# Kernel tuning notes

Measured on AMD Instinct MI355X. Metric: run time of the kernel, lower is better.

The kernel has to match this reference:

```python
import jax, jax.numpy as jnp
import numpy as np

EMB = 256

def setup_inputs() -> dict:
    key = jax.random.key(0)
    ks = jax.random.split(key, 7)
    c = EMB
    x = jax.random.normal(ks[0], (4, c, 64, 64), dtype=jnp.float32)
    s = 1.0 / np.sqrt(c)
    Wq = jax.random.uniform(ks[1], (c, c), jnp.float32, -s, s)
    bq = jax.random.uniform(ks[2], (c,), jnp.float32, -s, s)
    Wk = jax.random.uniform(ks[3], (c, c), jnp.float32, -s, s)
    bk = jax.random.uniform(ks[4], (c,), jnp.float32, -s, s)
    Wv = jax.random.uniform(ks[5], (c, c), jnp.float32, -s, s)
    bv = jax.random.uniform(ks[6], (c,), jnp.float32, -s, s)
    return {"x": x, "Wq": Wq, "bq": bq, "Wk": Wk, "bk": bk, "Wv": Wv, "bv": bv}

def reference(x, Wq, bq, Wk, bk, Wv, bv):
    b, c, h, w = x.shape
    scale = jnp.sqrt(jnp.float32(c))
    # [b, n, c] tokens, n = h*w
    xt = x.reshape(b, c, h * w).transpose(0, 2, 1)
    q = jnp.einsum('bnc,dc->bnd', xt, Wq) + bq
    k = jnp.einsum('bnc,dc->bnd', xt, Wk) + bk
    v = jnp.einsum('bnc,dc->bnd', xt, Wv) + bv
    dist = jnp.einsum('bnd,bmd->bnm', q, k) / scale  # [b, n, n]
    dist = jax.nn.softmax(dist, axis=-1)
    mem = jnp.einsum('bnm,bmd->bnd', dist, v)  # [b, n, c]
    # Original: permute(0,1,2) is identity, then raw view(b,c,h,w) -> reshape
    return mem.reshape(b, c, h, w)
```

## Files before the change

kernel.cpp:

```cpp
#include <hip/hip_runtime.h>

typedef __attribute__((ext_vector_type(8))) short short8;
typedef __attribute__((ext_vector_type(4))) short short4_t;
typedef __attribute__((ext_vector_type(4))) float float4_t;
typedef __attribute__((ext_vector_type(16))) float float16_t;
typedef __attribute__((ext_vector_type(2))) int int2_t;

#define NTOK 4096
#define CDIM 256
#define BPB (NTOK * CDIM)
#define C1 0.0901684400555602f

__device__ inline float bf2f(short s) {
    return __uint_as_float(((unsigned)(unsigned short)s) << 16);
}
__device__ inline short f2bf(float f) {
    unsigned u = __float_as_uint(f);
    return (short)((u + 0x7fffu + ((u >> 16) & 1u)) >> 16);
}
__device__ inline int cvtpk_bf16(float lo, float hi) {
    int d;
    asm("v_cvt_pk_bf16_f32 %0, %1, %2" : "=v"(d) : "v"(lo), "v"(hi));
    return d;
}
__device__ inline void gl_lds16(const void* g, void* l) {
    __builtin_amdgcn_global_load_lds(
        (const __attribute__((address_space(1))) unsigned int*)g,
        (__attribute__((address_space(3))) unsigned int*)l, 16, 0, 0);
}

__global__ void sniff_dtype(const unsigned* __restrict__ x, int* __restrict__ flag) {
    __shared__ int cnt;
    if (threadIdx.x == 0) cnt = 0;
    __syncthreads();
    int local = 0;
    for (int i = threadIdx.x; i < 1024; i += 256) {
        unsigned e = (x[i] >> 7) & 0xffu;
        if (e >= 100u && e <= 140u) local++;
    }
    atomicAdd(&cnt, local);
    __syncthreads();
    if (threadIdx.x == 0) flag[0] = (cnt >= 512) ? 1 : 0;
}

__global__ __launch_bounds__(256) void wprep(
    const void* __restrict__ Wq, const void* __restrict__ Wk,
    const void* __restrict__ Wv, const int* __restrict__ flag,
    short* __restrict__ Wb)
{
    const int base = (blockIdx.x * 256 + threadIdx.x) * 8;
    const int wsel = base >> 16, off = base & 65535;
    const void* W = (wsel == 0) ? Wq : (wsel == 1) ? Wk : Wv;
    short8 v;
    if (flag[0]) {
        v = *(const short8*)((const short*)W + off);
    } else {
        const float* f = (const float*)W + off;
        float4 a = *(const float4*)f;
        float4 c4 = *(const float4*)(f + 4);
        v[0]=f2bf(a.x);  v[1]=f2bf(a.y);  v[2]=f2bf(a.z);  v[3]=f2bf(a.w);
        v[4]=f2bf(c4.x); v[5]=f2bf(c4.y); v[6]=f2bf(c4.z); v[7]=f2bf(c4.w);
    }
    *(short8*)(Wb + base) = v;
}

template <bool PIN>
__global__ __launch_bounds__(256, 4) void qkv8(
    const void* __restrict__ xv, const short* __restrict__ Wb,
    const void* __restrict__ bq, const void* __restrict__ bk,
    const void* __restrict__ bv,
    const int* __restrict__ flag, int b0,
    short* __restrict__ qbase, short* __restrict__ kbase,
    short* __restrict__ vtbase)
{
    int nt, bl, wsel;
    if (PIN) {
        const int bid = blockIdx.x;
        wsel = bid >> 8;
        const int rem = bid & 255;
        bl = rem & 3; nt = rem >> 2;
    } else { nt = blockIdx.x; wsel = blockIdx.y; bl = blockIdx.z; }
    const int b = b0 + bl;
    const int n0 = nt * 64;
    const int tid = threadIdx.x;
    const int w = tid >> 6, lane = tid & 63, l15 = lane & 15, qd = lane >> 4;
    const int isbf = flag[0];

    __shared__ short obuf[64 * 264];

    short8 af[8];
    {
        const int n = n0 + 16 * w + l15;
        if (isbf) {
            const short* xs = (const short*)xv + (size_t)b * (CDIM * NTOK) + n;
            #pragma unroll
            for (int s = 0; s < 8; ++s) {
                short8 v;
                #pragma unroll
                for (int e = 0; e < 8; ++e)
                    v[e] = xs[(s * 32 + qd * 8 + e) * NTOK];
                af[s] = v;
            }
        } else {
            const float* xf = (const float*)xv + (size_t)b * (CDIM * NTOK) + n;
            #pragma unroll
            for (int s = 0; s < 8; ++s) {
                short8 v;
                #pragma unroll
                for (int e = 0; e < 8; ++e)
                    v[e] = f2bf(xf[(s * 32 + qd * 8 + e) * NTOK]);
                af[s] = v;
            }
        }
    }

    const short* W = Wb + wsel * 65536;
    const void* bp = (wsel == 0) ? bq : (wsel == 1) ? bk : bv;

    short8 wv[8], wn[8];
    {
        const short* wr = W + l15 * 256 + qd * 8;
        #pragma unroll
        for (int s = 0; s < 8; ++s) wv[s] = *(const short8*)(wr + s * 32);
    }
    #pragma unroll 1
    for (int dg = 0; dg < 16; ++dg) {
        const int d = dg * 16 + l15;
        if (dg + 1 < 16) {
            const short* wr = W + (dg * 16 + 16 + l15) * 256 + qd * 8;
            #pragma unroll
            for (int s = 0; s < 8; ++s) wn[s] = *(const short8*)(wr + s * 32);
        }
        float4_t acc = {0.f, 0.f, 0.f, 0.f};
        #pragma unroll
        for (int s = 0; s < 8; ++s)
            acc = __builtin_amdgcn_mfma_f32_16x16x32_bf16(af[s], wv[s], acc, 0, 0, 0);
        const float bias = isbf ? bf2f(((const short*)bp)[d])
                                : ((const float*)bp)[d];
        if (wsel < 2) {
            #pragma unroll
            for (int r = 0; r < 4; ++r)
                obuf[(16 * w + 4 * qd + r) * 264 + d] = f2bf(acc[r] + bias);
        } else {
            #pragma unroll
            for (int r = 0; r < 4; ++r)
                obuf[d * 66 + (16 * w + 4 * qd + r)] = f2bf(acc[r] + bias);
        }
        #pragma unroll
        for (int s = 0; s < 8; ++s) wv[s] = wn[s];
    }
    __syncthreads();

    if (wsel == 0) {
        short* qdst = qbase + (size_t)bl * BPB;
        const int rl = tid >> 2;
        #pragma unroll
        for (int u = 0; u < 8; ++u) {
            const int cc = (tid & 3) + 4 * u;
            short8 vv = *(const short8*)&obuf[rl * 264 + cc * 8];
            *(short8*)(qdst + (size_t)(n0 + rl) * 256 + cc * 8) = vv;
        }
    } else if (wsel == 1) {
        short* kdst = kbase + (size_t)bl * BPB;
        const int rl = tid >> 2;
        const int tile = (n0 + rl) >> 5, rit = rl & 31;
        #pragma unroll
        for (int u = 0; u < 8; ++u) {
            const int ccp = (tid & 3) + 4 * u;
            const int cc  = ccp ^ rit;
            short8 vv = *(const short8*)&obuf[rl * 264 + cc * 8];
            *(short8*)(kdst + (size_t)tile * 8192 + rit * 256 + ccp * 8) = vv;
        }
    } else {
        short* vtdst = vtbase + (size_t)bl * BPB;
        const int d = tid;
        #pragma unroll
        for (int u = 0; u < 8; ++u) {
            short8 vv = *(const short8*)&obuf[d * 66 + u * 8];
            const int tile = (n0 >> 5) + (u >> 2), ck = u & 3;
            const int pos = ((d & 1) * 4 + ck) ^ ((d >> 1) & 7);
            *(short8*)(vtdst + (size_t)tile * 8192 + (d >> 1) * 64 + pos * 8) = vv;
        }
    }
}

__global__ __launch_bounds__(256, 2) void flash13(
    const short* __restrict__ qb, const short* __restrict__ kb,
    const short* __restrict__ vtb,
    float* __restrict__ pO, float* __restrict__ pl)
{
    const int bid = blockIdx.x;
    const int bl = bid & 3, half = (bid >> 2) & 3, qt = bid >> 4;
    const int q0 = qt * 128;
    const int tid = threadIdx.x;
    const int w = tid >> 6, lane = tid & 63, l31 = lane & 31, h = lane >> 5;

    __shared__ __align__(16) char smem[65536];
    short* kbufA = (short*)smem;
    short* vbufA = (short*)(smem + 32768);

    const short* Q  = qb  + (size_t)bl * BPB;
    const char*  Kc = (const char*)(kb  + (size_t)bl * BPB);
    const char*  Vc = (const char*)(vtb + (size_t)bl * BPB);

    short8 qf[16];
    {
        const short* qrow = Q + (size_t)(q0 + 32 * w + l31) * 256 + h * 8;
        #pragma unroll
        for (int s = 0; s < 16; ++s)
            qf[s] = *(const short8*)(qrow + s * 16);
    }

    float16_t oacc[8];
    #pragma unroll
    for (int dt = 0; dt < 8; ++dt)
        #pragma unroll
        for (int r = 0; r < 16; ++r) oacc[dt][r] = 0.f;
    float ll0 = 0.f, ll1 = 0.f, ll2 = 0.f, ll3 = 0.f;

    const int KT0 = half * 32, KT1 = KT0 + 32;

    {
        const char* ks = Kc + ((size_t)KT0 << 14);
        const char* vs = Vc + ((size_t)KT0 << 14);
        char* kd = smem + tid * 16;
        char* vd = smem + 32768 + tid * 16;
        #pragma unroll
        for (int u = 0; u < 4; ++u) {
            gl_lds16(ks + u * 4096 + tid * 16, kd + u * 4096);
            gl_lds16(vs + u * 4096 + tid * 16, vd + u * 4096);
        }
    }

    float16_t se, so;
    #pragma unroll
    for (int r = 0; r < 16; ++r) { se[r] = 0.f; so[r] = 0.f; }
    short8 pa0, pa1;

    #pragma unroll 1
    for (int kt = KT0; kt < KT1; ++kt) {
        if (kt > KT0) {
            #pragma unroll
            for (int r = 0; r < 16; ++r) se[r] = exp2f((se[r] + so[r]) * C1);
            #pragma unroll
            for (int g = 0; g < 4; ++g) {
                ll0 += se[4 * g + 0]; ll1 += se[4 * g + 1];
                ll2 += se[4 * g + 2]; ll3 += se[4 * g + 3];
            }
            {
                int x0 = cvtpk_bf16(se[0], se[1]);
                int y0 = cvtpk_bf16(se[4], se[5]);
                int z0 = cvtpk_bf16(se[2], se[3]);
                int u0 = cvtpk_bf16(se[6], se[7]);
                int2_t r1 = __builtin_amdgcn_permlane32_swap(x0, y0, false, false);
                int2_t r2 = __builtin_amdgcn_permlane32_swap(z0, u0, false, false);
                union { int i[4]; short8 s8; } uu;
                uu.i[0] = r1[0]; uu.i[1] = r2[0]; uu.i[2] = r1[1]; uu.i[3] = r2[1];
                pa0 = uu.s8;
                int x1 = cvtpk_bf16(se[8],  se[9]);
                int y1 = cvtpk_bf16(se[12], se[13]);
                int z1 = cvtpk_bf16(se[10], se[11]);
                int u1 = cvtpk_bf16(se[14], se[15]);
                int2_t r3 = __builtin_amdgcn_permlane32_swap(x1, y1, false, false);
                int2_t r4 = __builtin_amdgcn_permlane32_swap(z1, u1, false, false);
                union { int i[4]; short8 s8; } vv;
                vv.i[0] = r3[0]; vv.i[1] = r4[0]; vv.i[2] = r3[1]; vv.i[3] = r4[1];
                pa1 = vv.s8;
            }
            {
                const short* vprev = vbufA + ((kt + 1) & 1) * 8192;
                __builtin_amdgcn_s_setprio(1);
                #pragma unroll
                for (int dt = 0; dt < 8; ++dt) {
                    const int d = 32 * dt + l31, d2 = d >> 1;
                    {
                        const int pos = (((d & 1) * 4 + h) ^ (d2 & 7));
                        short8 vf = *(const short8*)&vprev[d2 * 64 + pos * 8];
                        oacc[dt] = __builtin_amdgcn_mfma_f32_32x32x16_bf16(pa0, vf, oacc[dt], 0, 0, 0);
                    }
                    {
                        const int pos = (((d & 1) * 4 + 2 + h) ^ (d2 & 7));
                        short8 vf = *(const short8*)&vprev[d2 * 64 + pos * 8];
                        oacc[dt] = __builtin_amdgcn_mfma_f32_32x32x16_bf16(pa1, vf, oacc[dt], 0, 0, 0);
                    }
                }
                __builtin_amdgcn_s_setprio(0);
            }
        }

        asm volatile("s_waitcnt vmcnt(0) lgkmcnt(0)" ::: "memory");
        __builtin_amdgcn_sched_barrier(0);
        __builtin_amdgcn_s_barrier();
        __builtin_amdgcn_sched_barrier(0);

        if (kt + 1 < KT1) {
            const int alt = (kt + 1) & 1;
            const char* ks = Kc + ((size_t)(kt + 1) << 14);
            const char* vs = Vc + ((size_t)(kt + 1) << 14);
            char* kd = smem + alt * 16384 + tid * 16;
            char* vd = smem + 32768 + alt * 16384 + tid * 16;
            #pragma unroll
            for (int u = 0; u < 4; ++u) {
                gl_lds16(ks + u * 4096 + tid * 16, kd + u * 4096);
                gl_lds16(vs + u * 4096 + tid * 16, vd + u * 4096);
            }
        }

        {
            const short* kcur = kbufA + (kt & 1) * 8192;
            #pragma unroll
            for (int r = 0; r < 16; ++r) { se[r] = 0.f; so[r] = 0.f; }
            __builtin_amdgcn_s_setprio(1);
            #pragma unroll
            for (int j = 0; j < 8; ++j) {
                short8 ka = *(const short8*)
                    &kcur[l31 * 256 + (((4 * j + h) ^ l31) * 8)];
                se = __builtin_amdgcn_mfma_f32_32x32x16_bf16(ka, qf[2 * j], se, 0, 0, 0);
                short8 kb2 = *(const short8*)
                    &kcur[l31 * 256 + (((4 * j + 2 + h) ^ l31) * 8)];
                so = __builtin_amdgcn_mfma_f32_32x32x16_bf16(kb2, qf[2 * j + 1], so, 0, 0, 0);
            }
            __builtin_amdgcn_s_setprio(0);
        }
    }

    {
        #pragma unroll
        for (int r = 0; r < 16; ++r) se[r] = exp2f((se[r] + so[r]) * C1);
        #pragma unroll
        for (int g = 0; g < 4; ++g) {
            ll0 += se[4 * g + 0]; ll1 += se[4 * g + 1];
            ll2 += se[4 * g + 2]; ll3 += se[4 * g + 3];
        }
        int x0 = cvtpk_bf16(se[0], se[1]);
        int y0 = cvtpk_bf16(se[4], se[5]);
        int z0 = cvtpk_bf16(se[2], se[3]);
        int u0 = cvtpk_bf16(se[6], se[7]);
        int2_t r1 = __builtin_amdgcn_permlane32_swap(x0, y0, false, false);
        int2_t r2 = __builtin_amdgcn_permlane32_swap(z0, u0, false, false);
        union { int i[4]; short8 s8; } uu;
        uu.i[0] = r1[0]; uu.i[1] = r2[0]; uu.i[2] = r1[1]; uu.i[3] = r2[1];
        pa0 = uu.s8;
        int x1 = cvtpk_bf16(se[8],  se[9]);
        int y1 = cvtpk_bf16(se[12], se[13]);
        int z1 = cvtpk_bf16(se[10], se[11]);
        int u1 = cvtpk_bf16(se[14], se[15]);
        int2_t r3 = __builtin_amdgcn_permlane32_swap(x1, y1, false, false);
        int2_t r4 = __builtin_amdgcn_permlane32_swap(z1, u1, false, false);
        union { int i[4]; short8 s8; } vv;
        vv.i[0] = r3[0]; vv.i[1] = r4[0]; vv.i[2] = r3[1]; vv.i[3] = r4[1];
        pa1 = vv.s8;

        const short* vlast = vbufA + ((KT1 - 1) & 1) * 8192;
        #pragma unroll
        for (int dt = 0; dt < 8; ++dt) {
            const int d = 32 * dt + l31, d2 = d >> 1;
            {
                const int pos = (((d & 1) * 4 + h) ^ (d2 & 7));
                short8 vf = *(const short8*)&vlast[d2 * 64 + pos * 8];
                oacc[dt] = __builtin_amdgcn_mfma_f32_32x32x16_bf16(pa0, vf, oacc[dt], 0, 0, 0);
            }
            {
                const int pos = (((d & 1) * 4 + 2 + h) ^ (d2 & 7));
                short8 vf = *(const short8*)&vlast[d2 * 64 + pos * 8];
                oacc[dt] = __builtin_amdgcn_mfma_f32_32x32x16_bf16(pa1, vf, oacc[dt], 0, 0, 0);
            }
        }
    }

    const size_t idx = (size_t)(bl * 32 + qt) * 4 + half;
    {
        float v2 = (ll0 + ll1) + (ll2 + ll3);
        v2 += __shfl_xor(v2, 32, 64);
        if (h == 0) pl[idx * 128 + 32 * w + l31] = v2;
    }
    float* po = pO + idx * 32768;
    #pragma unroll
    for (int dt = 0; dt < 8; ++dt) {
        #pragma unroll
        for (int r = 0; r < 16; ++r) {
            const int qrow = 32 * w + (r & 3) + 8 * (r >> 2) + 4 * h;
            po[qrow * 256 + 32 * dt + l31] = oacc[dt][r];
        }
    }
}

__global__ __launch_bounds__(256) void combine4(
    const float* __restrict__ pO, const float* __restrict__ pl,
    const int* __restrict__ flag, void* __restrict__ outv)
{
    const int tid = threadIdx.x, w = tid >> 6, lane = tid & 63;
    const int isbf = flag[0];
    #pragma unroll 1
    for (int st = 0; st < 16; ++st) {
        const int row = blockIdx.x * 64 + st * 4 + w;
        const int bl = row >> 12, n = row & 4095;
        const int qt = n >> 7, prow = n & 127;
        const size_t bidx = (size_t)(bl * 32 + qt) * 4;
        const float* P0 = pO + bidx * 32768 + prow * 256 + lane * 4;
        float4 a = *(const float4*)P0;
        float4 b = *(const float4*)(P0 + 32768);
        float4 c = *(const float4*)(P0 + 65536);
        float4 d = *(const float4*)(P0 + 98304);
        const float inv = 1.0f /
            (pl[(bidx + 0) * 128 + prow] + pl[(bidx + 1) * 128 + prow] +
             pl[(bidx + 2) * 128 + prow] + pl[(bidx + 3) * 128 + prow]);
        float4 r;
        r.x = (a.x + b.x + c.x + d.x) * inv;
        r.y = (a.y + b.y + c.y + d.y) * inv;
        r.z = (a.z + b.z + c.z + d.z) * inv;
        r.w = (a.w + b.w + c.w + d.w) * inv;
        const size_t o = (size_t)row * 256 + lane * 4;
        if (isbf) {
            short4_t pk;
            pk[0] = f2bf(r.x); pk[1] = f2bf(r.y);
            pk[2] = f2bf(r.z); pk[3] = f2bf(r.w);
            *(short4_t*)((short*)outv + o) = pk;
        } else {
            *(float4*)((float*)outv + o) = r;
        }
    }
}

template <bool PIN, bool SPLIT>
__global__ __launch_bounds__(256, 2) void flash12(
    int b0, const short* __restrict__ qb, const short* __restrict__ kb,
    const short* __restrict__ vtb, const int* __restrict__ flag,
    void* __restrict__ outv, float* __restrict__ pO, float* __restrict__ pl)
{
    int qt, bl, half;
    if (SPLIT) {
        const int bid = blockIdx.x;
        bl = (bid >> 1) & 3; half = bid & 1; qt = bid >> 3;
    } else if (PIN) {
        bl = blockIdx.x & 3; qt = blockIdx.x >> 2; half = 0;
    } else { qt = blockIdx.x; bl = blockIdx.z; half = 0; }

    const int b = b0 + bl;
    const int q0 = qt * 64;
    const int tid = threadIdx.x;
    const int w = tid >> 6, lane = tid & 63, l31 = lane & 31, h = lane >> 5;
    const int wi = w & 1, wh = w >> 1;

    __shared__ __align__(16) char smem[67584];
    short* kbufA = (short*)smem;
    short* vbufA = (short*)(smem + 32768);
    float* lbuf  = (float*)(smem + 66560);

    const short* Q  = qb  + (size_t)bl * BPB;
    const char*  Kc = (const char*)(kb  + (size_t)bl * BPB);
    const char*  Vc = (const char*)(vtb + (size_t)bl * BPB);

    short8 qf[16];
    {
        const short* qrow = Q + (size_t)(q0 + 32 * wh + l31) * 256 + h * 8;
        #pragma unroll
        for (int s = 0; s < 16; ++s)
            qf[s] = *(const short8*)(qrow + s * 16);
    }

    float16_t oacc[4];
    #pragma unroll
    for (int dt = 0; dt < 4; ++dt)
        #pragma unroll
        for (int r = 0; r < 16; ++r) oacc[dt][r] = 0.f;
    float ll0 = 0.f, ll1 = 0.f, ll2 = 0.f, ll3 = 0.f;

    const int KT0 = SPLIT ? half * 64 : 0;
    const int KT1 = KT0 + (SPLIT ? 64 : 128);

    {
        const char* ks = Kc + ((size_t)KT0 << 14);
        const char* vs = Vc + ((size_t)KT0 << 14);
        char* kd = smem + tid * 16;
        char* vd = smem + 32768 + tid * 16;
        #pragma unroll
        for (int u = 0; u < 4; ++u) {
            gl_lds16(ks + u * 4096 + tid * 16, kd + u * 4096);
            gl_lds16(vs + u * 4096 + tid * 16, vd + u * 4096);
        }
    }
    __syncthreads();

    short8 pa0 = {0,0,0,0,0,0,0,0}, pa1 = {0,0,0,0,0,0,0,0};

    #pragma unroll 1
    for (int kt = KT0; kt < KT1; ++kt) {
        short* kcur  = kbufA + (kt & 1) * 8192;
        short* vprev = vbufA + ((kt + 1) & 1) * 8192;

        if (kt + 1 < KT1) {
            const char* ks = Kc + ((size_t)(kt + 1) << 14);
            char* kd = smem + (((kt + 1) & 1) << 14) + tid * 16;
            #pragma unroll
            for (int u = 0; u < 4; ++u)
                gl_lds16(ks + u * 4096 + tid * 16, kd + u * 4096);
        }

        float16_t se, so;
        #pragma unroll
        for (int r = 0; r < 16; ++r) { se[r] = 0.f; so[r] = 0.f; }
        #pragma unroll
        for (int j = 0; j < 8; ++j) {
            short8 ka = *(const short8*)
                &kcur[l31 * 256 + (((4 * j + h) ^ l31) * 8)];
            se = __builtin_amdgcn_mfma_f32_32x32x16_bf16(ka, qf[2 * j], se, 0, 0, 0);
            short8 kb2 = *(const short8*)
                &kcur[l31 * 256 + (((4 * j + 2 + h) ^ l31) * 8)];
            so = __builtin_amdgcn_mfma_f32_32x32x16_bf16(kb2, qf[2 * j + 1], so, 0, 0, 0);
        }

        if (kt > KT0) {
            #pragma unroll
            for (int dt = 0; dt < 4; ++dt) {
                const int d = 128 * wi + 32 * dt + l31, d2 = d >> 1;
                {
                    const int pos = (((d & 1) * 4 + h) ^ (d2 & 7));
                    short8 vf = *(const short8*)&vprev[d2 * 64 + pos * 8];
                    oacc[dt] = __builtin_amdgcn_mfma_f32_32x32x16_bf16(pa0, vf, oacc[dt], 0, 0, 0);
                }
                {
                    const int pos = (((d & 1) * 4 + 2 + h) ^ (d2 & 7));
                    short8 vf = *(const short8*)&vprev[d2 * 64 + pos * 8];
                    oacc[dt] = __builtin_amdgcn_mfma_f32_32x32x16_bf16(pa1, vf, oacc[dt], 0, 0, 0);
                }
            }
        }

        asm volatile("s_waitcnt lgkmcnt(0)" ::: "memory");
        __builtin_amdgcn_sched_barrier(0);
        __builtin_amdgcn_s_barrier();
        __builtin_amdgcn_sched_barrier(0);

        if (kt + 1 < KT1) {
            const char* vs = Vc + ((size_t)(kt + 1) << 14);
            char* vd = smem + 32768 + (((kt + 1) & 1) << 14) + tid * 16;
            #pragma unroll
            for (int u = 0; u < 4; ++u)
                gl_lds16(vs + u * 4096 + tid * 16, vd + u * 4096);
        }

        float pf[16];
        #pragma unroll
        for (int r = 0; r < 16; ++r) pf[r] = exp2f((se[r] + so[r]) * C1);
        #pragma unroll
        for (int g = 0; g < 4; ++g) {
            ll0 += pf[4 * g + 0]; ll1 += pf[4 * g + 1];
            ll2 += pf[4 * g + 2]; ll3 += pf[4 * g + 3];
        }
        {
            int x0 = cvtpk_bf16(pf[0], pf[1]);
            int y0 = cvtpk_bf16(pf[4], pf[5]);
            int z0 = cvtpk_bf16(pf[2], pf[3]);
            int u0 = cvtpk_bf16(pf[6], pf[7]);
            int2_t r1 = __builtin_amdgcn_permlane32_swap(x0, y0, false, false);
            int2_t r2 = __builtin_amdgcn_permlane32_swap(z0, u0, false, false);
            union { int i[4]; short8 s8; } uu;
            uu.i[0] = r1[0]; uu.i[1] = r2[0]; uu.i[2] = r1[1]; uu.i[3] = r2[1];
            pa0 = uu.s8;
            int x1 = cvtpk_bf16(pf[8],  pf[9]);
            int y1 = cvtpk_bf16(pf[12], pf[13]);
            int z1 = cvtpk_bf16(pf[10], pf[11]);
            int u1 = cvtpk_bf16(pf[14], pf[15]);
            int2_t r3 = __builtin_amdgcn_permlane32_swap(x1, y1, false, false);
            int2_t r4 = __builtin_amdgcn_permlane32_swap(z1, u1, false, false);
            union { int i[4]; short8 s8; } vv;
            vv.i[0] = r3[0]; vv.i[1] = r4[0]; vv.i[2] = r3[1]; vv.i[3] = r4[1];
            pa1 = vv.s8;
        }

        __syncthreads();
    }

    {
        short* vlast = vbufA + 8192;
        #pragma unroll
        for (int dt = 0; dt < 4; ++dt) {
            const int d = 128 * wi + 32 * dt + l31, d2 = d >> 1;
            {
                const int pos = (((d & 1) * 4 + h) ^ (d2 & 7));
                short8 vf = *(const short8*)&vlast[d2 * 64 + pos * 8];
                oacc[dt] = __builtin_amdgcn_mfma_f32_32x32x16_bf16(pa0, vf, oacc[dt], 0, 0, 0);
            }
            {
                const int pos = (((d & 1) * 4 + 2 + h) ^ (d2 & 7));
                short8 vf = *(const short8*)&vlast[d2 * 64 + pos * 8];
                oacc[dt] = __builtin_amdgcn_mfma_f32_32x32x16_bf16(pa1, vf, oacc[dt], 0, 0, 0);
            }
        }
    }

    {
        float v2 = (ll0 + ll1) + (ll2 + ll3);
        v2 += __shfl_xor(v2, 32, 64);
        if (h == 0 && wi == 0) lbuf[32 * wh + l31] = v2;
    }

    if (SPLIT) {
        const size_t pidx = (size_t)(bl * 64 + qt) * 2 + half;
        float* po = pO + pidx * 16384;
        #pragma unroll
        for (int dt = 0; dt < 4; ++dt) {
            const int dim = 128 * wi + 32 * dt + l31;
            #pragma unroll
            for (int r = 0; r < 16; ++r) {
                const int qrow = 32 * wh + (r & 3) + 8 * (r >> 2) + 4 * h;
                po[qrow * 256 + dim] = oacc[dt][r];
            }
        }
        __syncthreads();
        if (tid < 64) pl[pidx * 64 + tid] = lbuf[tid];
    } else {
        __syncthreads();
        float* obuf = (float*)smem;
        #pragma unroll
        for (int dt = 0; dt < 4; ++dt) {
            const int dim = 128 * wi + 32 * dt + l31;
            #pragma unroll
            for (int r = 0; r < 16; ++r) {
                const int qrow = 32 * wh + (r & 3) + 8 * (r >> 2) + 4 * h;
                obuf[qrow * 260 + dim] = oacc[dt][r];
            }
        }
        __syncthreads();
        {
            const int row = tid >> 2, q4 = (tid & 3) * 64;
            const float inv = 1.0f / lbuf[row];
            const float* src = obuf + row * 260 + q4;
            const size_t o = (size_t)(b * NTOK + q0 + row) * 256 + q4;
            if (flag[0]) {
                short* op = (short*)outv;
                #pragma unroll
                for (int g = 0; g < 4; ++g) {
                    float4 a  = *(const float4*)(src + g * 8);
                    float4 c4 = *(const float4*)(src + g * 8 + 4);
                    short8 pk;
                    pk[0]=f2bf(a.x*inv);  pk[1]=f2bf(a.y*inv);
                    pk[2]=f2bf(a.z*inv);  pk[3]=f2bf(a.w*inv);
                    pk[4]=f2bf(c4.x*inv); pk[5]=f2bf(c4.y*inv);
                    pk[6]=f2bf(c4.z*inv); pk[7]=f2bf(c4.w*inv);
                    *(short8*)(op + o + g * 8) = pk;
                }
            } else {
                float* op = (float*)outv;
                #pragma unroll
                for (int g = 0; g < 16; ++g) {
                    float4 a = *(const float4*)(src + g * 4);
                    a.x *= inv; a.y *= inv; a.z *= inv; a.w *= inv;
                    *(float4*)(op + o + g * 4) = a;
                }
            }
        }
    }
}

__global__ __launch_bounds__(256) void combine2(
    const float* __restrict__ pO, const float* __restrict__ pl,
    const int* __restrict__ flag, void* __restrict__ outv)
{
    const int tile = blockIdx.x, tid = threadIdx.x;
    const int row = tid >> 2, seg = (tid & 3) * 64;
    const float* A = pO + (size_t)tile * 32768 + row * 256 + seg;
    const float* B = A + 16384;
    const float inv = 1.0f / (pl[tile * 128 + row] + pl[tile * 128 + 64 + row]);
    const size_t o = ((size_t)tile * 64 + row) * 256 + seg;
    if (flag[0]) {
        short* op = (short*)outv;
        #pragma unroll
        for (int g = 0; g < 8; ++g) {
            float4 a  = *(const float4*)(A + g * 8);
            float4 a2 = *(const float4*)(A + g * 8 + 4);
            float4 c  = *(const float4*)(B + g * 8);
            float4 c2 = *(const float4*)(B + g * 8 + 4);
            short8 pk;
            pk[0]=f2bf((a.x+c.x)*inv);   pk[1]=f2bf((a.y+c.y)*inv);
            pk[2]=f2bf((a.z+c.z)*inv);   pk[3]=f2bf((a.w+c.w)*inv);
            pk[4]=f2bf((a2.x+c2.x)*inv); pk[5]=f2bf((a2.y+c2.y)*inv);
            pk[6]=f2bf((a2.z+c2.z)*inv); pk[7]=f2bf((a2.w+c2.w)*inv);
            *(short8*)(op + o + g * 8) = pk;
        }
    } else {
        float* op = (float*)outv;
        #pragma unroll
        for (int g = 0; g < 16; ++g) {
            float4 a = *(const float4*)(A + g * 4);
            float4 c = *(const float4*)(B + g * 4);
            a.x = (a.x + c.x) * inv; a.y = (a.y + c.y) * inv;
            a.z = (a.z + c.z) * inv; a.w = (a.w + c.w) * inv;
            *(float4*)(op + o + g * 4) = a;
        }
    }
}

extern "C" void kernel_launch(void* const* d_in, const int* in_sizes, int n_in,
                              void* d_out, int out_size, void* d_ws, size_t ws_size,
                              hipStream_t stream)
{
    const size_t HDR = 256;
    const size_t WBB = 393216;
    const size_t TB  = (size_t)BPB * 2;
    const size_t OFF_K = HDR + WBB;
    const size_t need_prim = OFF_K + 12 * TB;
    const size_t PO2 = 33554432;
    const size_t need_s2 = need_prim + PO2 + 131072;
    const size_t PO4 = 67108864;
    const size_t need_s4 = need_prim + PO4 + 262144;

    int*   flag = (int*)d_ws;
    short* Wb   = (short*)((char*)d_ws + HDR);

    sniff_dtype<<<1, 256, 0, stream>>>((const unsigned*)d_in[0], flag);
    wprep<<<96, 256, 0, stream>>>(d_in[1], d_in[3], d_in[5], flag, Wb);

    if (ws_size >= need_prim) {
        short* kbase  = (short*)((char*)d_ws + OFF_K);
        short* vtbase = kbase  + 4 * (size_t)BPB;
        short* qbase  = vtbase + 4 * (size_t)BPB;
        qkv8<true><<<dim3(768, 1, 1), 256, 0, stream>>>(
            d_in[0], Wb, d_in[2], d_in[4], d_in[6], flag, 0,
            qbase, kbase, vtbase);
        if (ws_size >= need_s4) {
            float* pO = (float*)((char*)d_ws + need_prim);
            float* pl = (float*)((char*)d_ws + need_prim + PO4);
            flash13<<<dim3(512, 1, 1), 256, 0, stream>>>(
                qbase, kbase, vtbase, pO, pl);
            combine4<<<dim3(256, 1, 1), 256, 0, stream>>>(pO, pl, flag, d_out);
        } else if (ws_size >= need_s2) {
            float* pO = (float*)((char*)d_ws + need_prim);
            float* pl = (float*)((char*)d_ws + need_prim + PO2);
            flash12<true, true><<<dim3(512, 1, 1), 256, 0, stream>>>(
                0, qbase, kbase, vtbase, flag, d_out, pO, pl);
            combine2<<<dim3(256, 1, 1), 256, 0, stream>>>(pO, pl, flag, d_out);
        } else {
            flash12<true, false><<<dim3(256, 1, 1), 256, 0, stream>>>(
                0, qbase, kbase, vtbase, flag, d_out, nullptr, nullptr);
        }
        return;
    }

    int nb = 4;
    while (nb > 1 && ws_size < OFF_K + (size_t)nb * 3 * TB) nb--;
    short* kbase  = (short*)((char*)d_ws + OFF_K);
    short* vtbase = kbase + (size_t)nb * BPB;
    short* qbase  = vtbase + (size_t)nb * BPB;

    for (int b0 = 0; b0 < 4; b0 += nb) {
        const int nbc = (4 - b0) < nb ? (4 - b0) : nb;
        qkv8<false><<<dim3(64, 3, nbc), 256, 0, stream>>>(
            d_in[0], Wb, d_in[2], d_in[4], d_in[6], flag, b0,
            qbase, kbase, vtbase);
        flash12<false, false><<<dim3(64, 1, nbc), 256, 0, stream>>>(
            b0, qbase, kbase, vtbase, flag, d_out, nullptr, nullptr);
    }
}
```

Before: 224.7 us.

## Add 8-way key split flash kernel with 512-thread blocks and fused dtype sniff

Merges the dtype-sniff kernel into the weight-prep kernel, which saves one launch. Adds a flash14 path that uses 512-thread blocks covering 256 query rows each, splits the keys eight ways with 16 tiles per block, and writes partial outputs that a new combine8 kernel reduces. It also removes the s_setprio hints and drops the 2-way split path. The cost is a much larger partial-output buffer (128MB) and heavier combine traffic. The path only runs if the workspace is big enough, otherwise the previous 4-way path is used.

```diff
diff --git a/kernel.cpp b/kernel.cpp
--- a/kernel.cpp
+++ b/kernel.cpp
@@ -29,30 +29,30 @@
         (__attribute__((address_space(3))) unsigned int*)l, 16, 0, 0);
 }
 
-__global__ void sniff_dtype(const unsigned* __restrict__ x, int* __restrict__ flag) {
-    __shared__ int cnt;
-    if (threadIdx.x == 0) cnt = 0;
+__global__ __launch_bounds__(256) void wprep2(
+    const void* __restrict__ Wq, const void* __restrict__ Wk,
+    const void* __restrict__ Wv, const unsigned* __restrict__ x,
+    int* __restrict__ flag, short* __restrict__ Wb)
+{
+    __shared__ int cs;
+    if (threadIdx.x == 0) cs = 0;
     __syncthreads();
     int local = 0;
     for (int i = threadIdx.x; i < 1024; i += 256) {
         unsigned e = (x[i] >> 7) & 0xffu;
         if (e >= 100u && e <= 140u) local++;
     }
-    atomicAdd(&cnt, local);
+    atomicAdd(&cs, local);
     __syncthreads();
-    if (threadIdx.x == 0) flag[0] = (cnt >= 512) ? 1 : 0;
-}
-
-__global__ __launch_bounds__(256) void wprep(
-    const void* __restrict__ Wq, const void* __restrict__ Wk,
-    const void* __restrict__ Wv, const int* __restrict__ flag,
-    short* __restrict__ Wb)
-{
+    const int isbf = (cs >= 512) ? 1 : 0;
+
+    if (blockIdx.x == 0 && threadIdx.x == 0) flag[0] = isbf;
+
     const int base = (blockIdx.x * 256 + threadIdx.x) * 8;
     const int wsel = base >> 16, off = base & 65535;
     const void* W = (wsel == 0) ? Wq : (wsel == 1) ? Wk : Wv;
     short8 v;
-    if (flag[0]) {
+    if (isbf) {
         v = *(const short8*)((const short*)W + off);
     } else {
         const float* f = (const float*)W + off;
@@ -184,14 +184,14 @@
     }
 }
 
-__global__ __launch_bounds__(256, 2) void flash13(
+__global__ __launch_bounds__(512, 4) void flash14(
     const short* __restrict__ qb, const short* __restrict__ kb,
     const short* __restrict__ vtb,
     float* __restrict__ pO, float* __restrict__ pl)
 {
     const int bid = blockIdx.x;
-    const int bl = bid & 3, half = (bid >> 2) & 3, qt = bid >> 4;
-    const int q0 = qt * 128;
+    const int bl = bid & 3, half = (bid >> 2) & 7, qt = bid >> 5;
+    const int q0 = qt * 256;
     const int tid = threadIdx.x;
     const int w = tid >> 6, lane = tid & 63, l31 = lane & 31, h = lane >> 5;
 
@@ -218,7 +218,7 @@
         for (int r = 0; r < 16; ++r) oacc[dt][r] = 0.f;
     float ll0 = 0.f, ll1 = 0.f, ll2 = 0.f, ll3 = 0.f;
 
-    const int KT0 = half * 32, KT1 = KT0 + 32;
+    const int KT0 = half * 16, KT1 = KT0 + 16;
 
     {
         const char* ks = Kc + ((size_t)KT0 << 14);
@@ -226,9 +226,9 @@
         char* kd = smem + tid * 16;
         char* vd = smem + 32768 + tid * 16;
         #pragma unroll
-        for (int u = 0; u < 4; ++u) {
-            gl_lds16(ks + u * 4096 + tid * 16, kd + u * 4096);
-            gl_lds16(vs + u * 4096 + tid * 16, vd + u * 4096);
+        for (int u = 0; u < 2; ++u) {
+            gl_lds16(ks + u * 8192 + tid * 16, kd + u * 8192);
+            gl_lds16(vs + u * 8192 + tid * 16, vd + u * 8192);
         }
     }
 
@@ -269,7 +269,6 @@
             }
             {
                 const short* vprev = vbufA + ((kt + 1) & 1) * 8192;
-                __builtin_amdgcn_s_setprio(1);
                 #pragma unroll
                 for (int dt = 0; dt < 8; ++dt) {
                     const int d = 32 * dt + l31, d2 = d >> 1;
@@ -284,7 +283,6 @@
                         oacc[dt] = __builtin_amdgcn_mfma_f32_32x32x16_bf16(pa1, vf, oacc[dt], 0, 0, 0);
                     }
                 }
-                __builtin_amdgcn_s_setprio(0);
             }
         }
 
@@ -300,9 +298,9 @@
             char* kd = smem + alt * 16384 + tid * 16;
             char* vd = smem + 32768 + alt * 16384 + tid * 16;
             #pragma unroll
-            for (int u = 0; u < 4; ++u) {
-                gl_lds16(ks + u * 4096 + tid * 16, kd + u * 4096);
-                gl_lds16(vs + u * 4096 + tid * 16, vd + u * 4096);
+            for (int u = 0; u < 2; ++u) {
+                gl_lds16(ks + u * 8192 + tid * 16, kd + u * 8192);
+                gl_lds16(vs + u * 8192 + tid * 16, vd + u * 8192);
             }
         }
 
@@ -310,7 +308,6 @@
             const short* kcur = kbufA + (kt & 1) * 8192;
             #pragma unroll
             for (int r = 0; r < 16; ++r) { se[r] = 0.f; so[r] = 0.f; }
-            __builtin_amdgcn_s_setprio(1);
             #pragma unroll
             for (int j = 0; j < 8; ++j) {
                 short8 ka = *(const short8*)
@@ -320,7 +317,6 @@
                     &kcur[l31 * 256 + (((4 * j + 2 + h) ^ l31) * 8)];
                 so = __builtin_amdgcn_mfma_f32_32x32x16_bf16(kb2, qf[2 * j + 1], so, 0, 0, 0);
             }
-            __builtin_amdgcn_s_setprio(0);
         }
     }
 
@@ -351,7 +347,240 @@
         vv.i[0] = r3[0]; vv.i[1] = r4[0]; vv.i[2] = r3[1]; vv.i[3] = r4[1];
         pa1 = vv.s8;
 
-        const short* vlast = vbufA + ((KT1 - 1) & 1) * 8192;
+        const short* vlast = vbufA + 8192;
+        #pragma unroll
+        for (int dt = 0; dt < 8; ++dt) {
+            const int d = 32 * dt + l31, d2 = d >> 1;
+            {
+                const int pos = (((d & 1) * 4 + h) ^ (d2 & 7));
+                short8 vf = *(const short8*)&vlast[d2 * 64 + pos * 8];
+                oacc[dt] = __builtin_amdgcn_mfma_f32_32x32x16_bf16(pa0, vf, oacc[dt], 0, 0, 0);
+            }
+            {
+                const int pos = (((d & 1) * 4 + 2 + h) ^ (d2 & 7));
+                short8 vf = *(const short8*)&vlast[d2 * 64 + pos * 8];
+                oacc[dt] = __builtin_amdgcn_mfma_f32_32x32x16_bf16(pa1, vf, oacc[dt], 0, 0, 0);
+            }
+        }
+    }
+
+    const int tile = bl * 16 + qt;
+    const size_t idx = (size_t)tile * 8 + half;
+    {
+        float v2 = (ll0 + ll1) + (ll2 + ll3);
+        v2 += __shfl_xor(v2, 32, 64);
+        if (h == 0) pl[idx * 256 + 32 * w + l31] = v2;
+    }
+    float* po = pO + idx * 65536;
+    #pragma unroll
+    for (int dt = 0; dt < 8; ++dt) {
+        #pragma unroll
+        for (int r = 0; r < 16; ++r) {
+            const int qrow = 32 * w + (r & 3) + 8 * (r >> 2) + 4 * h;
+            po[qrow * 256 + 32 * dt + l31] = oacc[dt][r];
+        }
+    }
+}
+
+__global__ __launch_bounds__(256) void combine8(
+    const float* __restrict__ pO, const float* __restrict__ pl,
+    const int* __restrict__ flag, void* __restrict__ outv)
+{
+    const int tid = threadIdx.x, w = tid >> 6, lane = tid & 63;
+    const int isbf = flag[0];
+    #pragma unroll 1
+    for (int st = 0; st < 8; ++st) {
+        const int row = blockIdx.x * 32 + st * 4 + w;
+        const int bl = row >> 12, n = row & 4095;
+        const int qt = n >> 8, prow = n & 255;
+        const size_t bidx = (size_t)(bl * 16 + qt) * 8;
+        const float* P0 = pO + bidx * 65536 + prow * 256 + lane * 4;
+        float4 r = *(const float4*)P0;
+        float lsum = pl[bidx * 256 + prow];
+        #pragma unroll
+        for (int j = 1; j < 8; ++j) {
+            float4 a = *(const float4*)(P0 + (size_t)j * 65536);
+            r.x += a.x; r.y += a.y; r.z += a.z; r.w += a.w;
+            lsum += pl[(bidx + j) * 256 + prow];
+        }
+        const float inv = 1.0f / lsum;
+        r.x *= inv; r.y *= inv; r.z *= inv; r.w *= inv;
+        const size_t o = (size_t)row * 256 + lane * 4;
+        if (isbf) {
+            short4_t pk;
+            pk[0] = f2bf(r.x); pk[1] = f2bf(r.y);
+            pk[2] = f2bf(r.z); pk[3] = f2bf(r.w);
+            *(short4_t*)((short*)outv + o) = pk;
+        } else {
+            *(float4*)((float*)outv + o) = r;
+        }
+    }
+}
+
+__global__ __launch_bounds__(256, 2) void flash13(
+    const short* __restrict__ qb, const short* __restrict__ kb,
+    const short* __restrict__ vtb,
+    float* __restrict__ pO, float* __restrict__ pl)
+{
+    const int bid = blockIdx.x;
+    const int bl = bid & 3, half = (bid >> 2) & 3, qt = bid >> 4;
+    const int q0 = qt * 128;
+    const int tid = threadIdx.x;
+    const int w = tid >> 6, lane = tid & 63, l31 = lane & 31, h = lane >> 5;
+
+    __shared__ __align__(16) char smem[65536];
+    short* kbufA = (short*)smem;
+    short* vbufA = (short*)(smem + 32768);
+
+    const short* Q  = qb  + (size_t)bl * BPB;
+    const char*  Kc = (const char*)(kb  + (size_t)bl * BPB);
+    const char*  Vc = (const char*)(vtb + (size_t)bl * BPB);
+
+    short8 qf[16];
+    {
+        const short* qrow = Q + (size_t)(q0 + 32 * w + l31) * 256 + h * 8;
+        #pragma unroll
+        for (int s = 0; s < 16; ++s)
+            qf[s] = *(const short8*)(qrow + s * 16);
+    }
+
+    float16_t oacc[8];
+    #pragma unroll
+    for (int dt = 0; dt < 8; ++dt)
+        #pragma unroll
+        for (int r = 0; r < 16; ++r) oacc[dt][r] = 0.f;
+    float ll0 = 0.f, ll1 = 0.f, ll2 = 0.f, ll3 = 0.f;
+
+    const int KT0 = half * 32, KT1 = KT0 + 32;
+
+    {
+        const char* ks = Kc + ((size_t)KT0 << 14);
+        const char* vs = Vc + ((size_t)KT0 << 14);
+        char* kd = smem + tid * 16;
+        char* vd = smem + 32768 + tid * 16;
+        #pragma unroll
+        for (int u = 0; u < 4; ++u) {
+            gl_lds16(ks + u * 4096 + tid * 16, kd + u * 4096);
+            gl_lds16(vs + u * 4096 + tid * 16, vd + u * 4096);
+        }
+    }
+
+    float16_t se, so;
+    #pragma unroll
+    for (int r = 0; r < 16; ++r) { se[r] = 0.f; so[r] = 0.f; }
+    short8 pa0, pa1;
+
+    #pragma unroll 1
+    for (int kt = KT0; kt < KT1; ++kt) {
+        if (kt > KT0) {
+            #pragma unroll
+            for (int r = 0; r < 16; ++r) se[r] = exp2f((se[r] + so[r]) * C1);
+            #pragma unroll
+            for (int g = 0; g < 4; ++g) {
+                ll0 += se[4 * g + 0]; ll1 += se[4 * g + 1];
+                ll2 += se[4 * g + 2]; ll3 += se[4 * g + 3];
+            }
+            {
+                int x0 = cvtpk_bf16(se[0], se[1]);
+                int y0 = cvtpk_bf16(se[4], se[5]);
+                int z0 = cvtpk_bf16(se[2], se[3]);
+                int u0 = cvtpk_bf16(se[6], se[7]);
+                int2_t r1 = __builtin_amdgcn_permlane32_swap(x0, y0, false, false);
+                int2_t r2 = __builtin_amdgcn_permlane32_swap(z0, u0, false, false);
+                union { int i[4]; short8 s8; } uu;
+                uu.i[0] = r1[0]; uu.i[1] = r2[0]; uu.i[2] = r1[1]; uu.i[3] = r2[1];
+                pa0 = uu.s8;
+                int x1 = cvtpk_bf16(se[8],  se[9]);
+                int y1 = cvtpk_bf16(se[12], se[13]);
+                int z1 = cvtpk_bf16(se[10], se[11]);
+                int u1 = cvtpk_bf16(se[14], se[15]);
+                int2_t r3 = __builtin_amdgcn_permlane32_swap(x1, y1, false, false);
+                int2_t r4 = __builtin_amdgcn_permlane32_swap(z1, u1, false, false);
+                union { int i[4]; short8 s8; } vv;
+                vv.i[0] = r3[0]; vv.i[1] = r4[0]; vv.i[2] = r3[1]; vv.i[3] = r4[1];
+                pa1 = vv.s8;
+            }
+            {
+                const short* vprev = vbufA + ((kt + 1) & 1) * 8192;
+                #pragma unroll
+                for (int dt = 0; dt < 8; ++dt) {
+                    const int d = 32 * dt + l31, d2 = d >> 1;
+                    {
+                        const int pos = (((d & 1) * 4 + h) ^ (d2 & 7));
+                        short8 vf = *(const short8*)&vprev[d2 * 64 + pos * 8];
+                        oacc[dt] = __builtin_amdgcn_mfma_f32_32x32x16_bf16(pa0, vf, oacc[dt], 0, 0, 0);
+                    }
+                    {
+                        const int pos = (((d & 1) * 4 + 2 + h) ^ (d2 & 7));
+                        short8 vf = *(const short8*)&vprev[d2 * 64 + pos * 8];
+                        oacc[dt] = __builtin_amdgcn_mfma_f32_32x32x16_bf16(pa1, vf, oacc[dt], 0, 0, 0);
+                    }
+                }
+            }
+        }
+
+        asm volatile("s_waitcnt vmcnt(0) lgkmcnt(0)" ::: "memory");
+        __builtin_amdgcn_sched_barrier(0);
+        __builtin_amdgcn_s_barrier();
+        __builtin_amdgcn_sched_barrier(0);
+
+        if (kt + 1 < KT1) {
+            const int alt = (kt + 1) & 1;
+            const char* ks = Kc + ((size_t)(kt + 1) << 14);
+            const char* vs = Vc + ((size_t)(kt + 1) << 14);
+            char* kd = smem + alt * 16384 + tid * 16;
+            char* vd = smem + 32768 + alt * 16384 + tid * 16;
+            #pragma unroll
+            for (int u = 0; u < 4; ++u) {
+                gl_lds16(ks + u * 4096 + tid * 16, kd + u * 4096);
+                gl_lds16(vs + u * 4096 + tid * 16, vd + u * 4096);
+            }
+        }
+
+        {
+            const short* kcur = kbufA + (kt & 1) * 8192;
+            #pragma unroll
+            for (int r = 0; r < 16; ++r) { se[r] = 0.f; so[r] = 0.f; }
+            #pragma unroll
+            for (int j = 0; j < 8; ++j) {
+                short8 ka = *(const short8*)
+                    &kcur[l31 * 256 + (((4 * j + h) ^ l31) * 8)];
+                se = __builtin_amdgcn_mfma_f32_32x32x16_bf16(ka, qf[2 * j], se, 0, 0, 0);
+                short8 kb2 = *(const short8*)
+                    &kcur[l31 * 256 + (((4 * j + 2 + h) ^ l31) * 8)];
+                so = __builtin_amdgcn_mfma_f32_32x32x16_bf16(kb2, qf[2 * j + 1], so, 0, 0, 0);
+            }
+        }
+    }
+
+    {
+        #pragma unroll
+        for (int r = 0; r < 16; ++r) se[r] = exp2f((se[r] + so[r]) * C1);
+        #pragma unroll
+        for (int g = 0; g < 4; ++g) {
+            ll0 += se[4 * g + 0]; ll1 += se[4 * g + 1];
+            ll2 += se[4 * g + 2]; ll3 += se[4 * g + 3];
+        }
+        int x0 = cvtpk_bf16(se[0], se[1]);
+        int y0 = cvtpk_bf16(se[4], se[5]);
+        int z0 = cvtpk_bf16(se[2], se[3]);
+        int u0 = cvtpk_bf16(se[6], se[7]);
+        int2_t r1 = __builtin_amdgcn_permlane32_swap(x0, y0, false, false);
+        int2_t r2 = __builtin_amdgcn_permlane32_swap(z0, u0, false, false);
+        union { int i[4]; short8 s8; } uu;
+        uu.i[0] = r1[0]; uu.i[1] = r2[0]; uu.i[2] = r1[1]; uu.i[3] = r2[1];
+        pa0 = uu.s8;
+        int x1 = cvtpk_bf16(se[8],  se[9]);
+        int y1 = cvtpk_bf16(se[12], se[13]);
+        int z1 = cvtpk_bf16(se[10], se[11]);
+        int u1 = cvtpk_bf16(se[14], se[15]);
+        int2_t r3 = __builtin_amdgcn_permlane32_swap(x1, y1, false, false);
+        int2_t r4 = __builtin_amdgcn_permlane32_swap(z1, u1, false, false);
+        union { int i[4]; short8 s8; } vv;
+        vv.i[0] = r3[0]; vv.i[1] = r4[0]; vv.i[2] = r3[1]; vv.i[3] = r4[1];
+        pa1 = vv.s8;
+
+        const short* vlast = vbufA + 8192;
         #pragma unroll
         for (int dt = 0; dt < 8; ++dt) {
             const int d = 32 * dt + l31, d2 = d >> 1;
@@ -422,19 +651,15 @@
     }
 }
 
-template <bool PIN, bool SPLIT>
+template <bool PIN>
 __global__ __launch_bounds__(256, 2) void flash12(
     int b0, const short* __restrict__ qb, const short* __restrict__ kb,
     const short* __restrict__ vtb, const int* __restrict__ flag,
-    void* __restrict__ outv, float* __restrict__ pO, float* __restrict__ pl)
+    void* __restrict__ outv)
 {
-    int qt, bl, half;
-    if (SPLIT) {
-        const int bid = blockIdx.x;
-        bl = (bid >> 1) & 3; half = bid & 1; qt = bid >> 3;
-    } else if (PIN) {
-        bl = blockIdx.x & 3; qt = blockIdx.x >> 2; half = 0;
-    } else { qt = blockIdx.x; bl = blockIdx.z; half = 0; }
+    int qt, bl;
+    if (PIN) { bl = blockIdx.x & 3; qt = blockIdx.x >> 2; }
+    else     { qt = blockIdx.x; bl = blockIdx.z; }
 
     const int b = b0 + bl;
     const int q0 = qt * 64;
@@ -466,12 +691,9 @@
         for (int r = 0; r < 16; ++r) oacc[dt][r] = 0.f;
     float ll0 = 0.f, ll1 = 0.f, ll2 = 0.f, ll3 = 0.f;
 
-    const int KT0 = SPLIT ? half * 64 : 0;
-    const int KT1 = KT0 + (SPLIT ? 64 : 128);
-
-    {
-        const char* ks = Kc + ((size_t)KT0 << 14);
-        const char* vs = Vc + ((size_t)KT0 << 14);
+    {
+        const char* ks = Kc;
+        const char* vs = Vc;
         char* kd = smem + tid * 16;
         char* vd = smem + 32768 + tid * 16;
         #pragma unroll
@@ -485,11 +707,11 @@
     short8 pa0 = {0,0,0,0,0,0,0,0}, pa1 = {0,0,0,0,0,0,0,0};
 
     #pragma unroll 1
-    for (int kt = KT0; kt < KT1; ++kt) {
+    for (int kt = 0; kt < 128; ++kt) {
         short* kcur  = kbufA + (kt & 1) * 8192;
         short* vprev = vbufA + ((kt + 1) & 1) * 8192;
 
-        if (kt + 1 < KT1) {
+        if (kt + 1 < 128) {
             const char* ks = Kc + ((size_t)(kt + 1) << 14);
             char* kd = smem + (((kt + 1) & 1) << 14) + tid * 16;
             #pragma unroll
@@ -510,7 +732,7 @@
             so = __builtin_amdgcn_mfma_f32_32x32x16_bf16(kb2, qf[2 * j + 1], so, 0, 0, 0);
         }
 
-        if (kt > KT0) {
+        if (kt > 0) {
             #pragma unroll
             for (int dt = 0; dt < 4; ++dt) {
                 const int d = 128 * wi + 32 * dt + l31, d2 = d >> 1;
@@ -532,7 +754,7 @@
         __builtin_amdgcn_s_barrier();
         __builtin_amdgcn_sched_barrier(0);
 
-        if (kt + 1 < KT1) {
+        if (kt + 1 < 128) {
             const char* vs = Vc + ((size_t)(kt + 1) << 14);
             char* vd = smem + 32768 + (((kt + 1) & 1) << 14) + tid * 16;
             #pragma unroll
@@ -596,98 +818,44 @@
         if (h == 0 && wi == 0) lbuf[32 * wh + l31] = v2;
     }
 
-    if (SPLIT) {
-        const size_t pidx = (size_t)(bl * 64 + qt) * 2 + half;
-        float* po = pO + pidx * 16384;
-        #pragma unroll
-        for (int dt = 0; dt < 4; ++dt) {
-            const int dim = 128 * wi + 32 * dt + l31;
-            #pragma unroll
-            for (int r = 0; r < 16; ++r) {
-                const int qrow = 32 * wh + (r & 3) + 8 * (r >> 2) + 4 * h;
-                po[qrow * 256 + dim] = oacc[dt][r];
-            }
-        }
-        __syncthreads();
-        if (tid < 64) pl[pidx * 64 + tid] = lbuf[tid];
-    } else {
-        __syncthreads();
-        float* obuf = (float*)smem;
-        #pragma unroll
-        for (int dt = 0; dt < 4; ++dt) {
-            const int dim = 128 * wi + 32 * dt + l31;
-            #pragma unroll
-            for (int r = 0; r < 16; ++r) {
-                const int qrow = 32 * wh + (r & 3) + 8 * (r >> 2) + 4 * h;
-                obuf[qrow * 260 + dim] = oacc[dt][r];
-            }
-        }
-        __syncthreads();
-        {
-            const int row = tid >> 2, q4 = (tid & 3) * 64;
-            const float inv = 1.0f / lbuf[row];
-            const float* src = obuf + row * 260 + q4;
-            const size_t o = (size_t)(b * NTOK + q0 + row) * 256 + q4;
-            if (flag[0]) {
-                short* op = (short*)outv;
-                #pragma unroll
-                for (int g = 0; g < 4; ++g) {
-                    float4 a  = *(const float4*)(src + g * 8);
-                    float4 c4 = *(const float4*)(src + g * 8 + 4);
-                    short8 pk;
-                    pk[0]=f2bf(a.x*inv);  pk[1]=f2bf(a.y*inv);
-                    pk[2]=f2bf(a.z*inv);  pk[3]=f2bf(a.w*inv);
-                    pk[4]=f2bf(c4.x*inv); pk[5]=f2bf(c4.y*inv);
-                    pk[6]=f2bf(c4.z*inv); pk[7]=f2bf(c4.w*inv);
-                    *(short8*)(op + o + g * 8) = pk;
-                }
-            } else {
-                float* op = (float*)outv;
-                #pragma unroll
-                for (int g = 0; g < 16; ++g) {
-                    float4 a = *(const float4*)(src + g * 4);
-                    a.x *= inv; a.y *= inv; a.z *= inv; a.w *= inv;
-                    *(float4*)(op + o + g * 4) = a;
-                }
-            }
-        }
-    }
-}
-
-__global__ __launch_bounds__(256) void combine2(
-    const float* __restrict__ pO, const float* __restrict__ pl,
-    const int* __restrict__ flag, void* __restrict__ outv)
-{
-    const int tile = blockIdx.x, tid = threadIdx.x;
-    const int row = tid >> 2, seg = (tid & 3) * 64;
-    const float* A = pO + (size_t)tile * 32768 + row * 256 + seg;
-    const float* B = A + 16384;
-    const float inv = 1.0f / (pl[tile * 128 + row] + pl[tile * 128 + 64 + row]);
-    const size_t o = ((size_t)tile * 64 + row) * 256 + seg;
-    if (flag[0]) {
-        short* op = (short*)outv;
-        #pragma unroll
-        for (int g = 0; g < 8; ++g) {
-            float4 a  = *(const float4*)(A + g * 8);
-            float4 a2 = *(const float4*)(A + g * 8 + 4);
-            float4 c  = *(const float4*)(B + g * 8);
-            float4 c2 = *(const float4*)(B + g * 8 + 4);
-            short8 pk;
-            pk[0]=f2bf((a.x+c.x)*inv);   pk[1]=f2bf((a.y+c.y)*inv);
-            pk[2]=f2bf((a.z+c.z)*inv);   pk[3]=f2bf((a.w+c.w)*inv);
-            pk[4]=f2bf((a2.x+c2.x)*inv); pk[5]=f2bf((a2.y+c2.y)*inv);
-            pk[6]=f2bf((a2.z+c2.z)*inv); pk[7]=f2bf((a2.w+c2.w)*inv);
-            *(short8*)(op + o + g * 8) = pk;
-        }
-    } else {
-        float* op = (float*)outv;
-        #pragma unroll
-        for (int g = 0; g < 16; ++g) {
-            float4 a = *(const float4*)(A + g * 4);
-            float4 c = *(const float4*)(B + g * 4);
-            a.x = (a.x + c.x) * inv; a.y = (a.y + c.y) * inv;
-            a.z = (a.z + c.z) * inv; a.w = (a.w + c.w) * inv;
-            *(float4*)(op + o + g * 4) = a;
+    __syncthreads();
+    float* obuf = (float*)smem;
+    #pragma unroll
+    for (int dt = 0; dt < 4; ++dt) {
+        const int dim = 128 * wi + 32 * dt + l31;
+        #pragma unroll
+        for (int r = 0; r < 16; ++r) {
+            const int qrow = 32 * wh + (r & 3) + 8 * (r >> 2) + 4 * h;
+            obuf[qrow * 260 + dim] = oacc[dt][r];
+        }
+    }
+    __syncthreads();
+    {
+        const int row = tid >> 2, q4 = (tid & 3) * 64;
+        const float inv = 1.0f / lbuf[row];
+        const float* src = obuf + row * 260 + q4;
+        const size_t o = (size_t)(b * NTOK + q0 + row) * 256 + q4;
+        if (flag[0]) {
+            short* op = (short*)outv;
+            #pragma unroll
+            for (int g = 0; g < 4; ++g) {
+                float4 a  = *(const float4*)(src + g * 8);
+                float4 c4 = *(const float4*)(src + g * 8 + 4);
+                short8 pk;
+                pk[0]=f2bf(a.x*inv);  pk[1]=f2bf(a.y*inv);
+                pk[2]=f2bf(a.z*inv);  pk[3]=f2bf(a.w*inv);
+                pk[4]=f2bf(c4.x*inv); pk[5]=f2bf(c4.y*inv);
+                pk[6]=f2bf(c4.z*inv); pk[7]=f2bf(c4.w*inv);
+                *(short8*)(op + o + g * 8) = pk;
+            }
+        } else {
+            float* op = (float*)outv;
+            #pragma unroll
+            for (int g = 0; g < 16; ++g) {
+                float4 a = *(const float4*)(src + g * 4);
+                a.x *= inv; a.y *= inv; a.z *= inv; a.w *= inv;
+                *(float4*)(op + o + g * 4) = a;
+            }
         }
     }
 }
@@ -696,21 +864,21 @@
                               void* d_out, int out_size, void* d_ws, size_t ws_size,
                               hipStream_t stream)
 {
-    const size_t HDR = 256;
+    const size_t HDR = 1024;
     const size_t WBB = 393216;
     const size_t TB  = (size_t)BPB * 2;
     const size_t OFF_K = HDR + WBB;
     const size_t need_prim = OFF_K + 12 * TB;
-    const size_t PO2 = 33554432;
-    const size_t need_s2 = need_prim + PO2 + 131072;
     const size_t PO4 = 67108864;
     const size_t need_s4 = need_prim + PO4 + 262144;
+    const size_t PO8 = 134217728;
+    const size_t need_s8 = need_prim + PO8 + 1048576;
 
     int*   flag = (int*)d_ws;
     short* Wb   = (short*)((char*)d_ws + HDR);
 
-    sniff_dtype<<<1, 256, 0, stream>>>((const unsigned*)d_in[0], flag);
-    wprep<<<96, 256, 0, stream>>>(d_in[1], d_in[3], d_in[5], flag, Wb);
+    wprep2<<<96, 256, 0, stream>>>(
+        d_in[1], d_in[3], d_in[5], (const unsigned*)d_in[0], flag, Wb);
 
     if (ws_size >= need_prim) {
         short* kbase  = (short*)((char*)d_ws + OFF_K);
@@ -719,21 +887,21 @@
         qkv8<true><<<dim3(768, 1, 1), 256, 0, stream>>>(
             d_in[0], Wb, d_in[2], d_in[4], d_in[6], flag, 0,
             qbase, kbase, vtbase);
-        if (ws_size >= need_s4) {
+        if (ws_size >= need_s8) {
+            float* pO = (float*)((char*)d_ws + need_prim);
+            float* pl = (float*)((char*)d_ws + need_prim + PO8);
+            flash14<<<dim3(512, 1, 1), 512, 0, stream>>>(
+                qbase, kbase, vtbase, pO, pl);
+            combine8<<<dim3(512, 1, 1), 256, 0, stream>>>(pO, pl, flag, d_out);
+        } else if (ws_size >= need_s4) {
             float* pO = (float*)((char*)d_ws + need_prim);
             float* pl = (float*)((char*)d_ws + need_prim + PO4);
             flash13<<<dim3(512, 1, 1), 256, 0, stream>>>(
                 qbase, kbase, vtbase, pO, pl);
             combine4<<<dim3(256, 1, 1), 256, 0, stream>>>(pO, pl, flag, d_out);
-        } else if (ws_size >= need_s2) {
-            float* pO = (float*)((char*)d_ws + need_prim);
-            float* pl = (float*)((char*)d_ws + need_prim + PO2);
-            flash12<true, true><<<dim3(512, 1, 1), 256, 0, stream>>>(
-                0, qbase, kbase, vtbase, flag, d_out, pO, pl);
-            combine2<<<dim3(256, 1, 1), 256, 0, stream>>>(pO, pl, flag, d_out);
         } else {
-            flash12<true, false><<<dim3(256, 1, 1), 256, 0, stream>>>(
-                0, qbase, kbase, vtbase, flag, d_out, nullptr, nullptr);
+            flash12<true><<<dim3(256, 1, 1), 256, 0, stream>>>(
+                0, qbase, kbase, vtbase, flag, d_out);
         }
         return;
     }
@@ -749,7 +917,7 @@
         qkv8<false><<<dim3(64, 3, nbc), 256, 0, stream>>>(
             d_in[0], Wb, d_in[2], d_in[4], d_in[6], flag, b0,
             qbase, kbase, vtbase);
-        flash12<false, false><<<dim3(64, 1, nbc), 256, 0, stream>>>(
-            b0, qbase, kbase, vtbase, flag, d_out, nullptr, nullptr);
-    }
-}
+        flash12<false><<<dim3(64, 1, nbc), 256, 0, stream>>>(
+            b0, qbase, kbase, vtbase, flag, d_out);
+    }
+}
```

New measurement: 885.1 us. 294% more time.
